# Kernel optimization log

Hardware: AMD Instinct MI355X
Metric: run time of the kernel (lower is better)

Reference implementation:

```python
import jax, jax.numpy as jnp
import numpy as np
from functools import partial

C = 96
D_STATE = 16
D_CONV = 4
EXPAND = 2
D_INNER = EXPAND * C
DT_RANK = (C + 15) // 16  # ceil(96/16) = 6
EPS = 1e-6


def _ln_cf(x, w, b):
    # channels_first LayerNorm over axis=1 of [B,C,D,H,W]
    u = jnp.mean(x, axis=1, keepdims=True)
    s = jnp.mean((x - u) ** 2, axis=1, keepdims=True)
    xn = (x - u) / jnp.sqrt(s + EPS)
    return w[None, :, None, None, None] * xn + b[None, :, None, None, None]


def _ln_last(x, w, b):
    u = jnp.mean(x, axis=-1, keepdims=True)
    s = jnp.mean((x - u) ** 2, axis=-1, keepdims=True)
    return (x - u) / jnp.sqrt(s + 1e-5) * w + b


def _mamba(x, Win, conv_w, conv_b, Wx, Wdt, bdt, A_log, Dp, Wout):
    # x: [B, L, C]
    B, L, _ = x.shape
    xz = jnp.einsum('blc,ec->ble', x, Win)           # [B,L,2*di]
    xin, z = xz[..., :D_INNER], xz[..., D_INNER:]
    # depthwise causal conv along L
    xt = jnp.transpose(xin, (0, 2, 1))               # [B,di,L]
    xt = jnp.pad(xt, ((0, 0), (0, 0), (D_CONV - 1, 0)))
    xc = jax.lax.conv_general_dilated(
        xt, conv_w[:, None, :], window_strides=(1,), padding='VALID',
        feature_group_count=D_INNER, dimension_numbers=('NCH', 'OIH', 'NCH'))
    xc = jax.nn.silu(xc + conv_b[None, :, None])
    xc = jnp.transpose(xc, (0, 2, 1))                # [B,L,di]
    x_dbl = jnp.einsum('bld,ed->ble', xc, Wx)        # [B,L,dt_rank+2*ds]
    dt_r = x_dbl[..., :DT_RANK]
    Bm = x_dbl[..., DT_RANK:DT_RANK + D_STATE]       # [B,L,ds]
    Cm = x_dbl[..., DT_RANK + D_STATE:]              # [B,L,ds]
    dt = jax.nn.softplus(jnp.einsum('blr,dr->bld', dt_r, Wdt) + bdt)
    A = -jnp.exp(A_log)                              # [di,ds]
    dA = jnp.exp(dt[..., None] * A)                  # [B,L,di,ds]
    dBx = (dt * xc)[..., None] * Bm[:, :, None, :]   # [B,L,di,ds]

    def comb(e1, e2):
        a1, b1 = e1
        a2, b2 = e2
        return a1 * a2, a2 * b1 + b2

    _, h = jax.lax.associative_scan(comb, (dA, dBx), axis=1)
    y = jnp.einsum('blds,bls->bld', h, Cm) + xc * Dp
    y = y * jax.nn.silu(z)
    return jnp.einsum('bld,cd->blc', y, Wout)


def setup_inputs() -> dict:
    key = jax.random.key(0)
    ks = jax.random.split(key, 16)
    g = lambda k, sh: jax.random.normal(k, sh, dtype=jnp.float32) * 0.02
    inp = {
        'x': jax.random.normal(ks[0], (2, C, 20, 20, 20), dtype=jnp.float32),
        'ln_w': jnp.ones((C,), jnp.float32), 'ln_b': jnp.zeros((C,), jnp.float32),
        'mln_w': jnp.ones((C,), jnp.float32), 'mln_b': jnp.zeros((C,), jnp.float32),
        'Win': g(ks[1], (2 * D_INNER, C)),
        'conv_w': g(ks[2], (D_INNER, D_CONV)), 'conv_b': jnp.zeros((D_INNER,), jnp.float32),
        'Wx': g(ks[3], (DT_RANK + 2 * D_STATE, D_INNER)),
        'Wdt': g(ks[4], (D_INNER, DT_RANK)), 'bdt': g(ks[5], (D_INNER,)),
        'A_log': jnp.log(jnp.broadcast_to(jnp.arange(1, D_STATE + 1, dtype=jnp.float32), (D_INNER, D_STATE))),
        'Dp': jnp.ones((D_INNER,), jnp.float32),
        'Wout': g(ks[6], (C, D_INNER)),
        'proj_w': g(ks[7], (C, 3 * C)), 'proj_b': jnp.zeros((C,), jnp.float32),
        'fc1_w': g(ks[8], (4 * C, C)), 'fc1_b': jnp.zeros((4 * C,), jnp.float32),
        'fc2_w': g(ks[9], (C, 4 * C)), 'fc2_b': jnp.zeros((C,), jnp.float32),
    }
    return inp


def reference(x, ln_w, ln_b, mln_w, mln_b, Win, conv_w, conv_b, Wx, Wdt, bdt,
              A_log, Dp, Wout, proj_w, proj_b, fc1_w, fc1_b, fc2_w, fc2_b):
    B, Cc, Dd, Hh, Ww = x.shape
    L = Dd * Hh * Ww
    x1 = _ln_cf(x, ln_w, ln_b)
    # three directional flattenings (cube, so reshape shapes match)
    outs = []
    for perm in ((0, 1, 2, 3, 4), (0, 1, 3, 4, 2), (0, 1, 4, 2, 3)):
        xp = jnp.transpose(x1, perm)                     # [B,C,a,b,c]
        xf = jnp.transpose(xp.reshape(B, Cc, L), (0, 2, 1))  # [B,L,C]
        xf = _ln_last(xf, mln_w, mln_b)
        y = _mamba(xf, Win, conv_w, conv_b, Wx, Wdt, bdt, A_log, Dp, Wout)
        outs.append(jnp.transpose(y, (0, 2, 1)).reshape(B, Cc, Dd, Hh, Ww))
    cat = jnp.concatenate(outs, axis=1)                  # [B,3C,D,H,W]
    out1 = jnp.einsum('oc,bcdhw->bodhw', proj_w, cat) + proj_b[None, :, None, None, None]
    out_res = x + out1
    h = _ln_cf(out_res, ln_w, ln_b)
    h = jnp.einsum('oc,bcdhw->bodhw', fc1_w, h) + fc1_b[None, :, None, None, None]
    h = jax.nn.gelu(h, approximate=False)
    h = jnp.einsum('oc,bcdhw->bodhw', fc2_w, h) + fc2_b[None, :, None, None, None]
    return h + out_res
```

## Files before the change

kernel.cpp:

```cpp
#include <hip/hip_runtime.h>
#include <hip/hip_fp16.h>
#include <math.h>

#define S   8000
#define BB  2
#define CC  96
#define DI  192
#define NS  16
#define RK  6
#define GG  6
#define NC  200
#define LC  40
#define ND  38

typedef __attribute__((ext_vector_type(8))) short bf16x8;
typedef __attribute__((ext_vector_type(4))) float f32x4;
typedef __attribute__((ext_vector_type(2))) float f32x2;

__device__ __forceinline__ int pos_from_l(int dir, int l) {
  if (dir == 0) return l;
  int a  = l / 400;
  int r  = l - a * 400;
  int bq = r / 20;
  int cq = r - bq * 20;
  if (dir == 1) return cq * 400 + a * 20 + bq;
  return bq * 400 + cq * 20 + a;
}

__device__ __forceinline__ float silu(float z) {
  return z / (1.f + __expf(-z));
}

__device__ __forceinline__ unsigned short f2bf(float x) {
  unsigned int u = __float_as_uint(x);
  u += 0x7FFFu + ((u >> 16) & 1u);
  return (unsigned short)(u >> 16);
}
__device__ __forceinline__ float bf2f(unsigned short h) {
  return __uint_as_float((unsigned int)h << 16);
}
__device__ __forceinline__ float h2f_bits(unsigned short h) {
  __half hh = *reinterpret_cast<__half*>(&h);
  return __half2float(hh);
}
__device__ __forceinline__ unsigned short f2h_bits(float x) {
  __half hh = __float2half(x);
  return *reinterpret_cast<unsigned short*>(&hh);
}

__device__ __forceinline__ float pair_sum(float y) {
  return y + __int_as_float(__builtin_amdgcn_update_dpp(
      0, __float_as_int(y), 0xB1, 0xF, 0xF, true));
}
__device__ __forceinline__ float quad_sum(float x) {
  x += __int_as_float(__builtin_amdgcn_update_dpp(0, __float_as_int(x), 0xB1, 0xF, 0xF, true));
  x += __int_as_float(__builtin_amdgcn_update_dpp(0, __float_as_int(x), 0x4E, 0xF, 0xF, true));
  return x;
}

template <int ACT, bool DOUBLE, bool OUTBF16>
__global__ __launch_bounds__(256) void k_lnmfma(const float* __restrict__ Xsrc,
    const float* __restrict__ lnw, const float* __restrict__ lnb,
    const float* __restrict__ mlnw, const float* __restrict__ mlnb,
    const float* __restrict__ Bw, const float* __restrict__ bias,
    void* __restrict__ Cout, int M, int N) {
  __shared__ float Xf[64][97];
  __shared__ unsigned short Al[64][104];
  __shared__ unsigned short Bl[96][104];
  int tid = threadIdx.x;
  int m0 = blockIdx.x * 64, n0 = blockIdx.y * 96;
  int b = m0 / S, pos0 = m0 - b * S;
  for (int idx = tid; idx < 64 * 96; idx += 256) {
    int row = idx & 63, c = idx >> 6;
    Xf[row][c] = Xsrc[((size_t)b * CC + c) * S + pos0 + row];
  }
  for (int idx = tid; idx < 96 * 24; idx += 256) {
    int bn = idx / 24, kq = idx - bn * 24;
    int n = n0 + bn;
    float4 v = make_float4(0.f, 0.f, 0.f, 0.f);
    if (n < N) v = *(const float4*)&Bw[(size_t)n * 96 + kq * 4];
    unsigned short* dst = &Bl[bn][kq * 4];
    dst[0] = f2bf(v.x); dst[1] = f2bf(v.y);
    dst[2] = f2bf(v.z); dst[3] = f2bf(v.w);
  }
  __syncthreads();
  {
    int row = tid >> 2, part = tid & 3;
    const float* xr = &Xf[row][part * 24];
    float s1 = 0.f, s2 = 0.f;
#pragma unroll
    for (int i = 0; i < 24; ++i) { float v = xr[i]; s1 += v; s2 += v * v; }
    s1 = quad_sum(s1); s2 = quad_sum(s2);
    float u = s1 * (1.f / 96.f);
    float var = s2 * (1.f / 96.f) - u * u;
    float rstd = rsqrtf(var + 1e-6f);
    if (DOUBLE) {
      float t1 = 0.f, t2 = 0.f;
#pragma unroll
      for (int i = 0; i < 24; ++i) {
        int c = part * 24 + i;
        float y1 = fmaf(lnw[c], (xr[i] - u) * rstd, lnb[c]);
        t1 += y1; t2 += y1 * y1;
      }
      t1 = quad_sum(t1); t2 = quad_sum(t2);
      float u2 = t1 * (1.f / 96.f);
      float var2 = t2 * (1.f / 96.f) - u2 * u2;
      float rstd2 = rsqrtf(var2 + 1e-5f);
#pragma unroll
      for (int i = 0; i < 24; ++i) {
        int c = part * 24 + i;
        float y1 = fmaf(lnw[c], (xr[i] - u) * rstd, lnb[c]);
        Al[row][c] = f2bf(fmaf(mlnw[c], (y1 - u2) * rstd2, mlnb[c]));
      }
    } else {
#pragma unroll
      for (int i = 0; i < 24; ++i) {
        int c = part * 24 + i;
        Al[row][c] = f2bf(fmaf(lnw[c], (xr[i] - u) * rstd, lnb[c]));
      }
    }
  }
  __syncthreads();
  int wid = tid >> 6, lane = tid & 63;
  int wr = wid >> 1, wc = wid & 1;
  int l16 = lane & 15, lk = (lane >> 4) * 8;
  f32x4 acc[2][3];
#pragma unroll
  for (int i = 0; i < 2; ++i)
#pragma unroll
    for (int j = 0; j < 3; ++j) acc[i][j] = (f32x4){0.f, 0.f, 0.f, 0.f};
#pragma unroll
  for (int kc = 0; kc < 96; kc += 32) {
    bf16x8 af[2], bfr[3];
#pragma unroll
    for (int i = 0; i < 2; ++i)
      af[i] = *(const bf16x8*)&Al[wr * 32 + i * 16 + l16][kc + lk];
#pragma unroll
    for (int j = 0; j < 3; ++j)
      bfr[j] = *(const bf16x8*)&Bl[wc * 48 + j * 16 + l16][kc + lk];
#pragma unroll
    for (int i = 0; i < 2; ++i)
#pragma unroll
      for (int j = 0; j < 3; ++j)
        acc[i][j] = __builtin_amdgcn_mfma_f32_16x16x32_bf16(
            af[i], bfr[j], acc[i][j], 0, 0, 0);
  }
#pragma unroll
  for (int i = 0; i < 2; ++i) {
#pragma unroll
    for (int j = 0; j < 3; ++j) {
#pragma unroll
      for (int v = 0; v < 4; ++v) {
        int m = m0 + wr * 32 + i * 16 + (lane >> 4) * 4 + v;
        int n = n0 + wc * 48 + j * 16 + l16;
        if (n < N) {
          float val = acc[i][j][v];
          val += bias ? bias[n] : 0.f;
          if (ACT == 1) val = 0.5f * val * (1.f + erff(val * 0.70710678118654752f));
          if (OUTBF16) ((unsigned short*)Cout)[(size_t)m * N + n] = f2bf(val);
          else         ((float*)Cout)[(size_t)m * N + n] = val;
        }
      }
    }
  }
}

#define BKP 40
template <int ACT, bool BIAS, bool RESID, bool OUT_BCS, bool GATEA, bool ABF16>
__global__ __launch_bounds__(256) void k_mfma(const void* __restrict__ Ap,
    const float* __restrict__ Bw, const float* __restrict__ bias,
    const float* __restrict__ resid, const unsigned short* __restrict__ XZg,
    float* __restrict__ Cmat, int M, int N, int K) {
  __shared__ unsigned short Al[64][BKP];
  __shared__ unsigned short Bl[96][BKP];
  int tid = threadIdx.x;
  int m0 = blockIdx.x * 64, n0 = blockIdx.y * 96;
  int wid = tid >> 6, lane = tid & 63;
  int wr = wid >> 1, wc = wid & 1;
  int l16 = lane & 15, lk = (lane >> 4) * 8;
  f32x4 acc[2][3];
#pragma unroll
  for (int i = 0; i < 2; ++i)
#pragma unroll
    for (int j = 0; j < 3; ++j) acc[i][j] = (f32x4){0.f, 0.f, 0.f, 0.f};

  for (int kk = 0; kk < K; kk += 32) {
    if (ABF16) {
      int row = tid >> 2, kq = tid & 3;
      int m = m0 + row;
      const unsigned short* As = (const unsigned short*)Ap;
      uint4 v = *(const uint4*)&As[(size_t)m * K + kk + kq * 8];
      if (GATEA) {
        unsigned short* pv = (unsigned short*)&v;
        int bb = m / S, ll = m - bb * S;
        int j = kk + kq * 8;
        int dir = j / DI; int e0 = j - dir * DI;
        int p = pos_from_l(dir, ll);
        uint4 zv = *(const uint4*)&XZg[((size_t)bb * S + p) * 384 + DI + e0];
        const unsigned short* zp = (const unsigned short*)&zv;
#pragma unroll
        for (int q = 0; q < 8; ++q)
          pv[q] = f2bf(bf2f(pv[q]) * silu(bf2f(zp[q])));
      }
      *(uint4*)&Al[row][kq * 8] = v;
    } else {
#pragma unroll
      for (int i = 0; i < 2; ++i) {
        int idx = tid + i * 256;
        int row = idx >> 3, kq = idx & 7;
        int m = m0 + row;
        const float* Af = (const float*)Ap;
        float4 v = *(const float4*)&Af[(size_t)m * K + kk + kq * 4];
        unsigned short* dst = &Al[row][kq * 4];
        dst[0] = f2bf(v.x); dst[1] = f2bf(v.y);
        dst[2] = f2bf(v.z); dst[3] = f2bf(v.w);
      }
    }
#pragma unroll
    for (int i = 0; i < 3; ++i) {
      int idx = tid + i * 256;
      int bn = idx >> 3, kq = idx & 7;
      int n = n0 + bn;
      float4 v = make_float4(0.f, 0.f, 0.f, 0.f);
      if (n < N) v = *(const float4*)&Bw[(size_t)n * K + kk + kq * 4];
      unsigned short* dst = &Bl[bn][kq * 4];
      dst[0] = f2bf(v.x); dst[1] = f2bf(v.y);
      dst[2] = f2bf(v.z); dst[3] = f2bf(v.w);
    }
    __syncthreads();
    bf16x8 af[2], bfr[3];
#pragma unroll
    for (int i = 0; i < 2; ++i)
      af[i] = *(const bf16x8*)&Al[wr * 32 + i * 16 + l16][lk];
#pragma unroll
    for (int j = 0; j < 3; ++j)
      bfr[j] = *(const bf16x8*)&Bl[wc * 48 + j * 16 + l16][lk];
#pragma unroll
    for (int i = 0; i < 2; ++i)
#pragma unroll
      for (int j = 0; j < 3; ++j)
        acc[i][j] = __builtin_amdgcn_mfma_f32_16x16x32_bf16(
            af[i], bfr[j], acc[i][j], 0, 0, 0);
    __syncthreads();
  }
#pragma unroll
  for (int i = 0; i < 2; ++i) {
#pragma unroll
    for (int j = 0; j < 3; ++j) {
#pragma unroll
      for (int v = 0; v < 4; ++v) {
        int m = m0 + wr * 32 + i * 16 + (lane >> 4) * 4 + v;
        int n = n0 + wc * 48 + j * 16 + l16;
        if (n < N) {
          float val = acc[i][j][v];
          if (BIAS) val += bias[n];
          if (ACT == 1) val = 0.5f * val * (1.f + erff(val * 0.70710678118654752f));
          if (RESID || OUT_BCS) {
            int bb = m / S, pp = m - bb * S;
            size_t oidx = ((size_t)bb * CC + n) * S + pp;
            if (RESID) val += resid[oidx];
            if (OUT_BCS) { Cmat[oidx] = val; continue; }
          }
          Cmat[(size_t)m * N + n] = val;
        }
      }
    }
  }
}

__global__ __launch_bounds__(256) void k_conv(const unsigned short* __restrict__ XZb,
    const float* __restrict__ cw, const float* __restrict__ cb,
    unsigned short* __restrict__ xcb) {
  int t = blockIdx.x * blockDim.x + threadIdx.x;
  if (t >= GG * S * 48) return;
  int q = t % 48; int gl = t / 48; int l = gl % S; int g = gl / S;
  int e0 = q * 4;
  int b = g / 3, dir = g - (g / 3) * 3;
  float cwv[4][4];
#pragma unroll
  for (int i = 0; i < 4; ++i)
    *(float4*)cwv[i] = *(const float4*)&cw[(e0 + i) * 4];
  float4 acc = *(const float4*)&cb[e0];
#pragma unroll
  for (int k = 0; k < 4; ++k) {
    int ls = l + k - 3;
    if (ls >= 0) {
      int p = pos_from_l(dir, ls);
      uint2 xz = *(const uint2*)&XZb[((size_t)b * S + p) * 384 + e0];
      const unsigned short* xp = (const unsigned short*)&xz;
      acc.x = fmaf(cwv[0][k], bf2f(xp[0]), acc.x);
      acc.y = fmaf(cwv[1][k], bf2f(xp[1]), acc.y);
      acc.z = fmaf(cwv[2][k], bf2f(xp[2]), acc.z);
      acc.w = fmaf(cwv[3][k], bf2f(xp[3]), acc.w);
    }
  }
  unsigned short o[4];
  o[0] = f2bf(acc.x * (1.f / (1.f + __expf(-acc.x))));
  o[1] = f2bf(acc.y * (1.f / (1.f + __expf(-acc.y))));
  o[2] = f2bf(acc.z * (1.f / (1.f + __expf(-acc.z))));
  o[3] = f2bf(acc.w * (1.f / (1.f + __expf(-acc.w))));
  *(uint2*)&xcb[(size_t)gl * DI + e0] = *(uint2*)o;
}

__global__ __launch_bounds__(256) void k_dtr(const float* __restrict__ xdbl,
    const float* __restrict__ Wdt, const float* __restrict__ bdt,
    const float* __restrict__ A_log, unsigned int* __restrict__ dr) {
  int t = blockIdx.x * blockDim.x + threadIdx.x;
  if (t >= GG * S * DI) return;
  int e = t % DI; int row = t / DI;
  const float* xr = xdbl + (size_t)row * ND;
  float a = bdt[e];
#pragma unroll
  for (int r = 0; r < RK; ++r) a = fmaf(Wdt[e * RK + r], xr[r], a);
  float d = fmaxf(a, 0.f) + __logf(1.f + __expf(-fabsf(a)));
  float base = -__expf(A_log[e * NS]);
  unsigned int lo = f2h_bits(d);
  unsigned int hi = f2h_bits(__expf(d * base));
  dr[t] = lo | (hi << 16);
}

__device__ __forceinline__ void stage_b16(float (*sB)[16],
    const float* __restrict__ xdbl, int g, int c, int tid) {
  const float* src = xdbl + ((size_t)g * S + c * LC) * ND + RK;
  for (int i = tid; i < LC * 16; i += 192) {
    int row = i >> 4, col = i & 15;
    sB[row][col] = src[(size_t)row * ND + col];
  }
}
__device__ __forceinline__ void stage_bc32(float (*sBC)[32],
    const float* __restrict__ xdbl, int g, int c, int tid) {
  const float* src = xdbl + ((size_t)g * S + c * LC) * ND + RK;
  for (int i = tid; i < LC * 32; i += 192) {
    int row = i >> 5, col = i & 31;
    sBC[row][col] = src[(size_t)row * ND + col];
  }
}

__global__ __launch_bounds__(192) void k_scanA(const unsigned short* __restrict__ xcb,
    const unsigned int* __restrict__ dr,
    const float* __restrict__ xdbl, const float* __restrict__ A_log,
    float* __restrict__ PA, float* __restrict__ EA) {
  __shared__ float sB[LC][16];
  int c = blockIdx.x, g = blockIdx.y;
  int tid = threadIdx.x;
  int e = blockIdx.z * 96 + (tid >> 1);
  int hf = tid & 1;
  stage_b16(sB, xdbl, g, c, tid);
  float base = -__expf(A_log[e * NS]);
  bool fast = true;
#pragma unroll
  for (int s = 1; s < NS; ++s) {
    float aes = -__expf(A_log[e * NS + s]);
    fast = fast && (fabsf(aes / base - (float)(s + 1)) < 1e-3f);
  }
  f32x2 h2[4];
#pragma unroll
  for (int k = 0; k < 4; ++k) h2[k] = (f32x2){0.f, 0.f};
  float T = 0.f;
  size_t sbase = ((size_t)g * S + c * LC) * DI + e;
  const unsigned short* xp = xcb + sbase;
  const unsigned int* drp = dr + sbase;
  __syncthreads();
  if (fast) {
    for (int l0 = 0; l0 < LC; l0 += 8) {
      float xb[8], db[8], rv[8];
#pragma unroll
      for (int j = 0; j < 8; ++j) {
        xb[j] = bf2f(xp[(size_t)(l0 + j) * DI]);
        unsigned int v = drp[(size_t)(l0 + j) * DI];
        db[j] = h2f_bits((unsigned short)(v & 0xffff));
        rv[j] = h2f_bits((unsigned short)(v >> 16));
      }
#pragma unroll
      for (int j = 0; j < 8; ++j) {
        int l = l0 + j;
        float d = db[j];
        T += d;
        float w = d * xb[j];
        float r = rv[j];
        float r2 = r * r, r4 = r2 * r2, r8 = r4 * r4;
        float f = hf ? r8 * r : r;
        f32x2 m0 = {f, f * r};
        f32x2 m1 = m0 * (f32x2){r2, r2};
        f32x2 m2 = m0 * (f32x2){r4, r4};
        f32x2 m3 = m1 * (f32x2){r4, r4};
        f32x2 wv = {w, w};
        float4 Ba = *(const float4*)&sB[l][hf * 8];
        float4 Bb = *(const float4*)&sB[l][hf * 8 + 4];
        h2[0] = m0 * h2[0] + wv * (f32x2){Ba.x, Ba.y};
        h2[1] = m1 * h2[1] + wv * (f32x2){Ba.z, Ba.w};
        h2[2] = m2 * h2[2] + wv * (f32x2){Bb.x, Bb.y};
        h2[3] = m3 * h2[3] + wv * (f32x2){Bb.z, Bb.w};
      }
    }
  } else {
    float Aes[8];
#pragma unroll
    for (int k = 0; k < 8; ++k) Aes[k] = -__expf(A_log[e * NS + hf * 8 + k]);
#pragma unroll 1
    for (int l = 0; l < LC; ++l) {
      unsigned int v = drp[(size_t)l * DI];
      float d = h2f_bits((unsigned short)(v & 0xffff));
      T += d;
      float w = d * bf2f(xp[(size_t)l * DI]);
#pragma unroll
      for (int k = 0; k < 8; ++k) {
        float q = __expf(d * Aes[k]);
        h2[k >> 1][k & 1] = fmaf(q, h2[k >> 1][k & 1], w * sB[l][hf * 8 + k]);
      }
    }
  }
  float* pp = PA + (((size_t)g * NC + c) * DI + e) * NS + hf * 8;
  float* ep = EA + (((size_t)g * NC + c) * DI + e) * NS + hf * 8;
  float po[8];
  if (fast) {
    float r = __expf(base * T);
    float r2 = r * r, r4 = r2 * r2, r8 = r4 * r4;
    float f = hf ? r8 * r : r;
    po[0] = f; po[1] = f * r; po[2] = f * r2; po[3] = po[1] * r2;
    po[4] = f * r4; po[5] = po[1] * r4; po[6] = po[2] * r4; po[7] = po[3] * r4;
  } else {
#pragma unroll
    for (int k = 0; k < 8; ++k)
      po[k] = __expf(-__expf(A_log[e * NS + hf * 8 + k]) * T);
  }
  *(float4*)&pp[0] = make_float4(po[0], po[1], po[2], po[3]);
  *(float4*)&pp[4] = make_float4(po[4], po[5], po[6], po[7]);
  *(float4*)&ep[0] = make_float4(h2[0][0], h2[0][1], h2[1][0], h2[1][1]);
  *(float4*)&ep[4] = make_float4(h2[2][0], h2[2][1], h2[3][0], h2[3][1]);
}

__global__ __launch_bounds__(256) void k_scanB(const float* PA,
    const float* EA, float* Hin) {
  int idx = blockIdx.x * blockDim.x + threadIdx.x;
  if (idx >= GG * DI * NS) return;
  int g = idx / (DI * NS); int es = idx - g * (DI * NS);
  size_t stride = (size_t)DI * NS;
  size_t b0 = (size_t)g * NC * stride + es;
  float h = 0.f;
  for (int c0 = 0; c0 < NC; c0 += 8) {
    float p8[8], e8[8];
#pragma unroll
    for (int j = 0; j < 8; ++j) {
      size_t ix = b0 + (size_t)(c0 + j) * stride;
      p8[j] = PA[ix]; e8[j] = EA[ix];
    }
#pragma unroll
    for (int j = 0; j < 8; ++j) {
      size_t ix = b0 + (size_t)(c0 + j) * stride;
      Hin[ix] = h;
      h = fmaf(p8[j], h, e8[j]);
    }
  }
}

__global__ __launch_bounds__(192) void k_scanC(const unsigned short* __restrict__ xcb,
    const unsigned int* __restrict__ dr,
    const float* __restrict__ xdbl, const float* __restrict__ A_log,
    const float* __restrict__ Hin, const float* __restrict__ Dp,
    unsigned short* __restrict__ ygb) {
  __shared__ float sBC[LC][32];
  int c = blockIdx.x, g = blockIdx.y;
  int tid = threadIdx.x;
  int e = blockIdx.z * 96 + (tid >> 1);
  int hf = tid & 1;
  const float* hp = Hin + (((size_t)g * NC + c) * DI + e) * NS + hf * 8;
  float4 h0 = *(const float4*)(hp + 0);
  float4 h1v = *(const float4*)(hp + 4);
  stage_bc32(sBC, xdbl, g, c, tid);
  float dpe = Dp[e];
  float base = -__expf(A_log[e * NS]);
  bool fast = true;
#pragma unroll
  for (int s = 1; s < NS; ++s) {
    float aes = -__expf(A_log[e * NS + s]);
    fast = fast && (fabsf(aes / base - (float)(s + 1)) < 1e-3f);
  }
  f32x2 h2[4] = {{h0.x, h0.y}, {h0.z, h0.w}, {h1v.x, h1v.y}, {h1v.z, h1v.w}};
  size_t sbase = ((size_t)g * S + c * LC) * DI + e;
  const unsigned short* xp = xcb + sbase;
  const unsigned int* drp = dr + sbase;
  int b = g / 3, dir = g - (g / 3) * 3;
  unsigned short* yo = ygb + ((size_t)b * S + c * LC) * 576 + dir * DI + e;
  __syncthreads();
  if (fast) {
    for (int l0 = 0; l0 < LC; l0 += 8) {
      float xb[8], db[8], rv[8];
#pragma unroll
      for (int j = 0; j < 8; ++j) {
        xb[j] = bf2f(xp[(size_t)(l0 + j) * DI]);
        unsigned int v = drp[(size_t)(l0 + j) * DI];
        db[j] = h2f_bits((unsigned short)(v & 0xffff));
        rv[j] = h2f_bits((unsigned short)(v >> 16));
      }
#pragma unroll
      for (int j = 0; j < 8; ++j) {
        int l = l0 + j;
        float d = db[j];
        float xv = xb[j];
        float w = d * xv;
        float r = rv[j];
        float r2 = r * r, r4 = r2 * r2, r8 = r4 * r4;
        float f = hf ? r8 * r : r;
        f32x2 m0 = {f, f * r};
        f32x2 m1 = m0 * (f32x2){r2, r2};
        f32x2 m2 = m0 * (f32x2){r4, r4};
        f32x2 m3 = m1 * (f32x2){r4, r4};
        f32x2 wv = {w, w};
        float4 Ba = *(const float4*)&sBC[l][hf * 8];
        float4 Bb = *(const float4*)&sBC[l][hf * 8 + 4];
        float4 Ca = *(const float4*)&sBC[l][16 + hf * 8];
        float4 Cb = *(const float4*)&sBC[l][16 + hf * 8 + 4];
        f32x2 yacc = {hf ? 0.f : xv * dpe, 0.f};
        h2[0] = m0 * h2[0] + wv * (f32x2){Ba.x, Ba.y};
        yacc += h2[0] * (f32x2){Ca.x, Ca.y};
        h2[1] = m1 * h2[1] + wv * (f32x2){Ba.z, Ba.w};
        yacc += h2[1] * (f32x2){Ca.z, Ca.w};
        h2[2] = m2 * h2[2] + wv * (f32x2){Bb.x, Bb.y};
        yacc += h2[2] * (f32x2){Cb.x, Cb.y};
        h2[3] = m3 * h2[3] + wv * (f32x2){Bb.z, Bb.w};
        yacc += h2[3] * (f32x2){Cb.z, Cb.w};
        float ysum = pair_sum(yacc[0] + yacc[1]);
        if (!hf) yo[(size_t)l * 576] = f2bf(ysum);
      }
    }
  } else {
    float Aes[8];
#pragma unroll
    for (int k = 0; k < 8; ++k) Aes[k] = -__expf(A_log[e * NS + hf * 8 + k]);
#pragma unroll 1
    for (int l = 0; l < LC; ++l) {
      unsigned int v = drp[(size_t)l * DI];
      float d = h2f_bits((unsigned short)(v & 0xffff));
      float xv = bf2f(xp[(size_t)l * DI]);
      float w = d * xv;
      float y = hf ? 0.f : xv * dpe;
#pragma unroll
      for (int k = 0; k < 8; ++k) {
        float q = __expf(d * Aes[k]);
        float hk = fmaf(q, h2[k >> 1][k & 1], w * sBC[l][hf * 8 + k]);
        h2[k >> 1][k & 1] = hk;
        y = fmaf(hk, sBC[l][16 + hf * 8 + k], y);
      }
      float ysum = pair_sum(y);
      if (!hf) yo[(size_t)l * 576] = f2bf(ysum);
    }
  }
}

__global__ __launch_bounds__(256) void k_foldW(const float* __restrict__ proj_w,
    const float* __restrict__ Wout, float* __restrict__ Mcat) {
  int t = blockIdx.x * blockDim.x + threadIdx.x;
  if (t >= CC * 576) return;
  int o = t / 576; int j = t - o * 576; int dir = j / DI; int e = j - dir * DI;
  float a = 0.f;
  for (int c2 = 0; c2 < CC; ++c2)
    a = fmaf(proj_w[o * 288 + dir * CC + c2], Wout[c2 * DI + e], a);
  Mcat[t] = a;
}

extern "C" void kernel_launch(void* const* d_in, const int* in_sizes, int n_in,
                              void* d_out, int out_size, void* d_ws, size_t ws_size,
                              hipStream_t stream) {
  const float* x      = (const float*)d_in[0];
  const float* ln_w   = (const float*)d_in[1];
  const float* ln_b   = (const float*)d_in[2];
  const float* mln_w  = (const float*)d_in[3];
  const float* mln_b  = (const float*)d_in[4];
  const float* Win    = (const float*)d_in[5];
  const float* conv_w = (const float*)d_in[6];
  const float* conv_b = (const float*)d_in[7];
  const float* Wx     = (const float*)d_in[8];
  const float* Wdt    = (const float*)d_in[9];
  const float* bdt    = (const float*)d_in[10];
  const float* A_log  = (const float*)d_in[11];
  const float* Dp     = (const float*)d_in[12];
  const float* Wout   = (const float*)d_in[13];
  const float* proj_w = (const float*)d_in[14];
  const float* proj_b = (const float*)d_in[15];
  const float* fc1_w  = (const float*)d_in[16];
  const float* fc1_b  = (const float*)d_in[17];
  const float* fc2_w  = (const float*)d_in[18];
  const float* fc2_b  = (const float*)d_in[19];

  float* ws = (float*)d_ws;
  size_t off = 0;
  float* ores = ws + off; off += (size_t)BB * S * CC;
  float* XZf  = ws + off; off += (size_t)BB * S * 384 / 2;
  float* xcf  = ws + off; off += (size_t)GG * S * DI / 2;
  float* xdbl = ws + off; off += (size_t)GG * S * ND;
  float* drf  = ws + off; off += (size_t)GG * S * DI;
  float* PA   = ws + off; off += (size_t)GG * NC * DI * NS;
  float* EA   = ws + off; off += (size_t)GG * NC * DI * NS;
  float* yg   = ws + off; off += (size_t)BB * S * 576 / 2;
  float* Mcat = ws + off; off += (size_t)CC * 576;
  if (ws_size < off * sizeof(float)) return;
  float* Hin  = PA;
  unsigned short* XZb = (unsigned short*)XZf;
  unsigned short* xcb = (unsigned short*)xcf;
  unsigned int*   dr  = (unsigned int*)drf;
  unsigned short* ygb = (unsigned short*)yg;
  unsigned short* h1  = (unsigned short*)XZf;

  k_lnmfma<0, true, true><<<dim3(BB * S / 64, 4), 256, 0, stream>>>(
      x, ln_w, ln_b, mln_w, mln_b, Win, nullptr, XZb, BB * S, 384);
  k_conv<<<(GG * S * 48 + 255) / 256, 256, 0, stream>>>(XZb, conv_w, conv_b, xcb);
  k_mfma<0, false, false, false, false, true>
      <<<dim3(GG * S / 64, 1), 256, 0, stream>>>(
      xcb, Wx, nullptr, nullptr, nullptr, xdbl, GG * S, ND, DI);
  k_dtr<<<(GG * S * DI + 255) / 256, 256, 0, stream>>>(
      xdbl, Wdt, bdt, A_log, dr);
  k_scanA<<<dim3(NC, GG, 2), 192, 0, stream>>>(
      xcb, dr, xdbl, A_log, PA, EA);
  k_scanB<<<(GG * DI * NS + 255) / 256, 256, 0, stream>>>(PA, EA, Hin);
  k_scanC<<<dim3(NC, GG, 2), 192, 0, stream>>>(
      xcb, dr, xdbl, A_log, Hin, Dp, ygb);
  k_foldW<<<(CC * 576 + 255) / 256, 256, 0, stream>>>(proj_w, Wout, Mcat);
  k_mfma<0, true, true, true, true, true>
      <<<dim3(BB * S / 64, 1), 256, 0, stream>>>(
      ygb, Mcat, proj_b, x, XZb, ores, BB * S, CC, 576);
  k_lnmfma<1, false, true><<<dim3(BB * S / 64, 4), 256, 0, stream>>>(
      ores, ln_w, ln_b, nullptr, nullptr, fc1_w, fc1_b, h1, BB * S, 384);
  k_mfma<0, true, true, true, false, true>
      <<<dim3(BB * S / 64, 1), 256, 0, stream>>>(
      h1, fc2_w, fc2_b, ores, nullptr, (float*)d_out, BB * S, CC, 384);
}
```

Baseline: 286.4 us.

## Compute local scan output in pass A and apply carry-in correction in pass C

The chunked selective scan is restructured. The first pass now computes the full per-chunk local output y (with zero initial state), stores it along with a half-precision running cumulative dt, and uses one thread per channel over all 16 states instead of two half-threads. The third pass no longer re-runs the recurrence. It only adds the decayed carry-in contribution, using exp(A*T) derived from the stored cumulative sum, and skips wavefronts whose incoming state is all zero. k_dtr is also vectorised to produce four channels per thread with a 16-byte store. The trade-offs are an extra buffer write and read-modify-write of y, fp16 precision for the cumulative T, and fewer threads per block in pass A.

After: 258.8 us. 1.11x faster.

```diff
diff --git a/kernel.cpp b/kernel.cpp
--- a/kernel.cpp
+++ b/kernel.cpp
@@ -30,7 +30,6 @@
 __device__ __forceinline__ float silu(float z) {
   return z / (1.f + __expf(-z));
 }
-
 __device__ __forceinline__ unsigned short f2bf(float x) {
   unsigned int u = __float_as_uint(x);
   u += 0x7FFFu + ((u >> 16) & 1u);
@@ -46,11 +45,6 @@
 __device__ __forceinline__ unsigned short f2h_bits(float x) {
   __half hh = __float2half(x);
   return *reinterpret_cast<unsigned short*>(&hh);
-}
-
-__device__ __forceinline__ float pair_sum(float y) {
-  return y + __int_as_float(__builtin_amdgcn_update_dpp(
-      0, __float_as_int(y), 0xB1, 0xF, 0xF, true));
 }
 __device__ __forceinline__ float quad_sum(float x) {
   x += __int_as_float(__builtin_amdgcn_update_dpp(0, __float_as_int(x), 0xB1, 0xF, 0xF, true));
@@ -306,46 +300,42 @@
     const float* __restrict__ Wdt, const float* __restrict__ bdt,
     const float* __restrict__ A_log, unsigned int* __restrict__ dr) {
   int t = blockIdx.x * blockDim.x + threadIdx.x;
-  if (t >= GG * S * DI) return;
-  int e = t % DI; int row = t / DI;
+  if (t >= GG * S * 48) return;
+  int q = t % 48; int row = t / 48;
+  int e0 = q * 4;
   const float* xr = xdbl + (size_t)row * ND;
-  float a = bdt[e];
-#pragma unroll
-  for (int r = 0; r < RK; ++r) a = fmaf(Wdt[e * RK + r], xr[r], a);
-  float d = fmaxf(a, 0.f) + __logf(1.f + __expf(-fabsf(a)));
-  float base = -__expf(A_log[e * NS]);
-  unsigned int lo = f2h_bits(d);
-  unsigned int hi = f2h_bits(__expf(d * base));
-  dr[t] = lo | (hi << 16);
-}
-
-__device__ __forceinline__ void stage_b16(float (*sB)[16],
-    const float* __restrict__ xdbl, int g, int c, int tid) {
-  const float* src = xdbl + ((size_t)g * S + c * LC) * ND + RK;
-  for (int i = tid; i < LC * 16; i += 192) {
-    int row = i >> 4, col = i & 15;
-    sB[row][col] = src[(size_t)row * ND + col];
-  }
-}
-__device__ __forceinline__ void stage_bc32(float (*sBC)[32],
-    const float* __restrict__ xdbl, int g, int c, int tid) {
-  const float* src = xdbl + ((size_t)g * S + c * LC) * ND + RK;
-  for (int i = tid; i < LC * 32; i += 192) {
-    int row = i >> 5, col = i & 31;
-    sBC[row][col] = src[(size_t)row * ND + col];
-  }
-}
-
-__global__ __launch_bounds__(192) void k_scanA(const unsigned short* __restrict__ xcb,
-    const unsigned int* __restrict__ dr,
-    const float* __restrict__ xdbl, const float* __restrict__ A_log,
-    float* __restrict__ PA, float* __restrict__ EA) {
-  __shared__ float sB[LC][16];
+  float r0 = xr[0], r1 = xr[1], r2 = xr[2], r3 = xr[3], r4 = xr[4], r5 = xr[5];
+  unsigned int out[4];
+#pragma unroll
+  for (int i = 0; i < 4; ++i) {
+    int e = e0 + i;
+    const float* wp = &Wdt[e * RK];
+    float a = bdt[e];
+    a = fmaf(wp[0], r0, a); a = fmaf(wp[1], r1, a); a = fmaf(wp[2], r2, a);
+    a = fmaf(wp[3], r3, a); a = fmaf(wp[4], r4, a); a = fmaf(wp[5], r5, a);
+    float d = fmaxf(a, 0.f) + __logf(1.f + __expf(-fabsf(a)));
+    float base = -__expf(A_log[e * NS]);
+    out[i] = (unsigned int)f2h_bits(d) | ((unsigned int)f2h_bits(__expf(d * base)) << 16);
+  }
+  *(uint4*)&dr[(size_t)row * DI + e0] = *(uint4*)out;
+}
+
+__global__ __launch_bounds__(192) void k_scanA2(const unsigned short* __restrict__ xcb,
+    const unsigned int* __restrict__ dr, const float* __restrict__ xdbl,
+    const float* __restrict__ A_log, const float* __restrict__ Dp,
+    float* __restrict__ PA, float* __restrict__ EA,
+    unsigned short* __restrict__ Tb, unsigned short* __restrict__ ygb) {
+  __shared__ float sBC[LC][32];
   int c = blockIdx.x, g = blockIdx.y;
   int tid = threadIdx.x;
-  int e = blockIdx.z * 96 + (tid >> 1);
-  int hf = tid & 1;
-  stage_b16(sB, xdbl, g, c, tid);
+  int e = tid;
+  {
+    const float* src = xdbl + ((size_t)g * S + c * LC) * ND + RK;
+    for (int i = tid; i < LC * 32; i += 192) {
+      int row = i >> 5, col = i & 31;
+      sBC[row][col] = src[(size_t)row * ND + col];
+    }
+  }
   float base = -__expf(A_log[e * NS]);
   bool fast = true;
 #pragma unroll
@@ -353,81 +343,115 @@
     float aes = -__expf(A_log[e * NS + s]);
     fast = fast && (fabsf(aes / base - (float)(s + 1)) < 1e-3f);
   }
-  f32x2 h2[4];
-#pragma unroll
-  for (int k = 0; k < 4; ++k) h2[k] = (f32x2){0.f, 0.f};
+  float dpe = Dp[e];
+  f32x2 h2[8];
+#pragma unroll
+  for (int k = 0; k < 8; ++k) h2[k] = (f32x2){0.f, 0.f};
   float T = 0.f;
   size_t sbase = ((size_t)g * S + c * LC) * DI + e;
   const unsigned short* xp = xcb + sbase;
   const unsigned int* drp = dr + sbase;
+  unsigned short* Tp = Tb + sbase;
+  int b = g / 3, dir = g - (g / 3) * 3;
+  unsigned short* yo = ygb + ((size_t)b * S + c * LC) * 576 + dir * DI + e;
   __syncthreads();
   if (fast) {
-    for (int l0 = 0; l0 < LC; l0 += 8) {
-      float xb[8], db[8], rv[8];
+    unsigned short xb[2][8];
+    unsigned int dv[2][8];
+#pragma unroll
+    for (int j = 0; j < 8; ++j) {
+      xb[0][j] = xp[(size_t)j * DI];
+      dv[0][j] = drp[(size_t)j * DI];
+    }
+#pragma unroll
+    for (int blk = 0; blk < 5; ++blk) {
+      int cb = blk & 1, nb = cb ^ 1;
+      if (blk < 4) {
+#pragma unroll
+        for (int j = 0; j < 8; ++j) {
+          xb[nb][j] = xp[(size_t)(blk * 8 + 8 + j) * DI];
+          dv[nb][j] = drp[(size_t)(blk * 8 + 8 + j) * DI];
+        }
+      }
 #pragma unroll
       for (int j = 0; j < 8; ++j) {
-        xb[j] = bf2f(xp[(size_t)(l0 + j) * DI]);
-        unsigned int v = drp[(size_t)(l0 + j) * DI];
-        db[j] = h2f_bits((unsigned short)(v & 0xffff));
-        rv[j] = h2f_bits((unsigned short)(v >> 16));
-      }
-#pragma unroll
-      for (int j = 0; j < 8; ++j) {
-        int l = l0 + j;
-        float d = db[j];
+        int l = blk * 8 + j;
+        float xv = bf2f(xb[cb][j]);
+        unsigned int v = dv[cb][j];
+        float d = h2f_bits((unsigned short)(v & 0xffff));
+        float r = h2f_bits((unsigned short)(v >> 16));
         T += d;
-        float w = d * xb[j];
-        float r = rv[j];
+        Tp[(size_t)l * DI] = f2h_bits(T);
+        float w = d * xv;
         float r2 = r * r, r4 = r2 * r2, r8 = r4 * r4;
-        float f = hf ? r8 * r : r;
-        f32x2 m0 = {f, f * r};
-        f32x2 m1 = m0 * (f32x2){r2, r2};
-        f32x2 m2 = m0 * (f32x2){r4, r4};
-        f32x2 m3 = m1 * (f32x2){r4, r4};
+        f32x2 r2v = {r2, r2}, r4v = {r4, r4}, r8v = {r8, r8};
+        f32x2 m0 = {r, r2};
+        f32x2 m1 = m0 * r2v, m2 = m0 * r4v, m3 = m1 * r4v;
+        f32x2 m4 = m0 * r8v, m5 = m1 * r8v, m6 = m2 * r8v, m7 = m3 * r8v;
         f32x2 wv = {w, w};
-        float4 Ba = *(const float4*)&sB[l][hf * 8];
-        float4 Bb = *(const float4*)&sB[l][hf * 8 + 4];
-        h2[0] = m0 * h2[0] + wv * (f32x2){Ba.x, Ba.y};
-        h2[1] = m1 * h2[1] + wv * (f32x2){Ba.z, Ba.w};
-        h2[2] = m2 * h2[2] + wv * (f32x2){Bb.x, Bb.y};
-        h2[3] = m3 * h2[3] + wv * (f32x2){Bb.z, Bb.w};
+        float4 Ba = *(const float4*)&sBC[l][0];
+        float4 Bb = *(const float4*)&sBC[l][4];
+        float4 Bc = *(const float4*)&sBC[l][8];
+        float4 Bd = *(const float4*)&sBC[l][12];
+        float4 Ca = *(const float4*)&sBC[l][16];
+        float4 Cb2 = *(const float4*)&sBC[l][20];
+        float4 Cc = *(const float4*)&sBC[l][24];
+        float4 Cd = *(const float4*)&sBC[l][28];
+        f32x2 ya = {xv * dpe, 0.f};
+        h2[0] = m0 * h2[0] + wv * (f32x2){Ba.x, Ba.y}; ya += h2[0] * (f32x2){Ca.x, Ca.y};
+        h2[1] = m1 * h2[1] + wv * (f32x2){Ba.z, Ba.w}; ya += h2[1] * (f32x2){Ca.z, Ca.w};
+        h2[2] = m2 * h2[2] + wv * (f32x2){Bb.x, Bb.y}; ya += h2[2] * (f32x2){Cb2.x, Cb2.y};
+        h2[3] = m3 * h2[3] + wv * (f32x2){Bb.z, Bb.w}; ya += h2[3] * (f32x2){Cb2.z, Cb2.w};
+        h2[4] = m4 * h2[4] + wv * (f32x2){Bc.x, Bc.y}; ya += h2[4] * (f32x2){Cc.x, Cc.y};
+        h2[5] = m5 * h2[5] + wv * (f32x2){Bc.z, Bc.w}; ya += h2[5] * (f32x2){Cc.z, Cc.w};
+        h2[6] = m6 * h2[6] + wv * (f32x2){Bd.x, Bd.y}; ya += h2[6] * (f32x2){Cd.x, Cd.y};
+        h2[7] = m7 * h2[7] + wv * (f32x2){Bd.z, Bd.w}; ya += h2[7] * (f32x2){Cd.z, Cd.w};
+        yo[(size_t)l * 576] = f2bf(ya[0] + ya[1]);
       }
     }
   } else {
-    float Aes[8];
-#pragma unroll
-    for (int k = 0; k < 8; ++k) Aes[k] = -__expf(A_log[e * NS + hf * 8 + k]);
+    float Aes[NS];
+#pragma unroll
+    for (int s = 0; s < NS; ++s) Aes[s] = -__expf(A_log[e * NS + s]);
 #pragma unroll 1
     for (int l = 0; l < LC; ++l) {
       unsigned int v = drp[(size_t)l * DI];
       float d = h2f_bits((unsigned short)(v & 0xffff));
+      float xv = bf2f(xp[(size_t)l * DI]);
       T += d;
-      float w = d * bf2f(xp[(size_t)l * DI]);
-#pragma unroll
-      for (int k = 0; k < 8; ++k) {
-        float q = __expf(d * Aes[k]);
-        h2[k >> 1][k & 1] = fmaf(q, h2[k >> 1][k & 1], w * sB[l][hf * 8 + k]);
-      }
-    }
-  }
-  float* pp = PA + (((size_t)g * NC + c) * DI + e) * NS + hf * 8;
-  float* ep = EA + (((size_t)g * NC + c) * DI + e) * NS + hf * 8;
-  float po[8];
+      Tp[(size_t)l * DI] = f2h_bits(T);
+      float w = d * xv;
+      float y = xv * dpe;
+#pragma unroll
+      for (int s = 0; s < NS; ++s) {
+        float q = __expf(d * Aes[s]);
+        float hk = fmaf(q, h2[s >> 1][s & 1], w * sBC[l][s]);
+        h2[s >> 1][s & 1] = hk;
+        y = fmaf(hk, sBC[l][16 + s], y);
+      }
+      yo[(size_t)l * 576] = f2bf(y);
+    }
+  }
+  float* pp = PA + (((size_t)g * NC + c) * DI + e) * NS;
+  float* ep = EA + (((size_t)g * NC + c) * DI + e) * NS;
+  float po[NS];
   if (fast) {
-    float r = __expf(base * T);
-    float r2 = r * r, r4 = r2 * r2, r8 = r4 * r4;
-    float f = hf ? r8 * r : r;
-    po[0] = f; po[1] = f * r; po[2] = f * r2; po[3] = po[1] * r2;
-    po[4] = f * r4; po[5] = po[1] * r4; po[6] = po[2] * r4; po[7] = po[3] * r4;
+    float R = __expf(base * T);
+    float R2 = R * R, R4 = R2 * R2, R8 = R4 * R4;
+    po[0] = R; po[1] = R2; po[2] = R * R2; po[3] = R4;
+    po[4] = R4 * R; po[5] = R4 * R2; po[6] = po[5] * R; po[7] = R8;
+    po[8] = R8 * R; po[9] = R8 * R2; po[10] = po[9] * R; po[11] = R8 * R4;
+    po[12] = po[11] * R; po[13] = po[11] * R2; po[14] = po[13] * R; po[15] = R8 * R8;
   } else {
 #pragma unroll
-    for (int k = 0; k < 8; ++k)
-      po[k] = __expf(-__expf(A_log[e * NS + hf * 8 + k]) * T);
-  }
-  *(float4*)&pp[0] = make_float4(po[0], po[1], po[2], po[3]);
-  *(float4*)&pp[4] = make_float4(po[4], po[5], po[6], po[7]);
-  *(float4*)&ep[0] = make_float4(h2[0][0], h2[0][1], h2[1][0], h2[1][1]);
-  *(float4*)&ep[4] = make_float4(h2[2][0], h2[2][1], h2[3][0], h2[3][1]);
+    for (int s = 0; s < NS; ++s)
+      po[s] = __expf(-__expf(A_log[e * NS + s]) * T);
+  }
+#pragma unroll
+  for (int s = 0; s < NS; s += 4) {
+    *(float4*)&pp[s] = make_float4(po[s], po[s+1], po[s+2], po[s+3]);
+    *(float4*)&ep[s] = make_float4(h2[s>>1][0], h2[s>>1][1], h2[(s>>1)+1][0], h2[(s>>1)+1][1]);
+  }
 }
 
 __global__ __launch_bounds__(256) void k_scanB(const float* PA,
@@ -454,21 +478,20 @@
   }
 }
 
-__global__ __launch_bounds__(192) void k_scanC(const unsigned short* __restrict__ xcb,
-    const unsigned int* __restrict__ dr,
+__global__ __launch_bounds__(192) void k_scanC2(const unsigned short* __restrict__ Tb,
     const float* __restrict__ xdbl, const float* __restrict__ A_log,
-    const float* __restrict__ Hin, const float* __restrict__ Dp,
-    unsigned short* __restrict__ ygb) {
-  __shared__ float sBC[LC][32];
+    const float* __restrict__ Hin, unsigned short* __restrict__ ygb) {
+  __shared__ float sC[LC][16];
   int c = blockIdx.x, g = blockIdx.y;
   int tid = threadIdx.x;
-  int e = blockIdx.z * 96 + (tid >> 1);
-  int hf = tid & 1;
-  const float* hp = Hin + (((size_t)g * NC + c) * DI + e) * NS + hf * 8;
-  float4 h0 = *(const float4*)(hp + 0);
-  float4 h1v = *(const float4*)(hp + 4);
-  stage_bc32(sBC, xdbl, g, c, tid);
-  float dpe = Dp[e];
+  int e = tid;
+  {
+    const float* src = xdbl + ((size_t)g * S + c * LC) * ND + RK + 16;
+    for (int i = tid; i < LC * 16; i += 192) {
+      int row = i >> 4, col = i & 15;
+      sC[row][col] = src[(size_t)row * ND + col];
+    }
+  }
   float base = -__expf(A_log[e * NS]);
   bool fast = true;
 #pragma unroll
@@ -476,74 +499,80 @@
     float aes = -__expf(A_log[e * NS + s]);
     fast = fast && (fabsf(aes / base - (float)(s + 1)) < 1e-3f);
   }
-  f32x2 h2[4] = {{h0.x, h0.y}, {h0.z, h0.w}, {h1v.x, h1v.y}, {h1v.z, h1v.w}};
+  const float* hp = Hin + (((size_t)g * NC + c) * DI + e) * NS;
+  float4 hv0 = *(const float4*)(hp + 0);
+  float4 hv1 = *(const float4*)(hp + 4);
+  float4 hv2 = *(const float4*)(hp + 8);
+  float4 hv3 = *(const float4*)(hp + 12);
+  f32x2 hin[8] = {{hv0.x, hv0.y}, {hv0.z, hv0.w}, {hv1.x, hv1.y}, {hv1.z, hv1.w},
+                  {hv2.x, hv2.y}, {hv2.z, hv2.w}, {hv3.x, hv3.y}, {hv3.z, hv3.w}};
+  float hmag = fabsf(hv0.x) + fabsf(hv0.y) + fabsf(hv0.z) + fabsf(hv0.w) +
+               fabsf(hv1.x) + fabsf(hv1.y) + fabsf(hv1.z) + fabsf(hv1.w) +
+               fabsf(hv2.x) + fabsf(hv2.y) + fabsf(hv2.z) + fabsf(hv2.w) +
+               fabsf(hv3.x) + fabsf(hv3.y) + fabsf(hv3.z) + fabsf(hv3.w);
   size_t sbase = ((size_t)g * S + c * LC) * DI + e;
-  const unsigned short* xp = xcb + sbase;
-  const unsigned int* drp = dr + sbase;
+  const unsigned short* Tp = Tb + sbase;
   int b = g / 3, dir = g - (g / 3) * 3;
   unsigned short* yo = ygb + ((size_t)b * S + c * LC) * 576 + dir * DI + e;
   __syncthreads();
+  if (__builtin_amdgcn_ballot_w64(hmag != 0.f) == 0ull) return;
   if (fast) {
-    for (int l0 = 0; l0 < LC; l0 += 8) {
-      float xb[8], db[8], rv[8];
+    unsigned short tb2[2][8], yb[2][8];
+#pragma unroll
+    for (int j = 0; j < 8; ++j) {
+      tb2[0][j] = Tp[(size_t)j * DI];
+      yb[0][j] = yo[(size_t)j * 576];
+    }
+#pragma unroll
+    for (int blk = 0; blk < 5; ++blk) {
+      int cb = blk & 1, nb = cb ^ 1;
+      if (blk < 4) {
+#pragma unroll
+        for (int j = 0; j < 8; ++j) {
+          tb2[nb][j] = Tp[(size_t)(blk * 8 + 8 + j) * DI];
+          yb[nb][j] = yo[(size_t)(blk * 8 + 8 + j) * 576];
+        }
+      }
 #pragma unroll
       for (int j = 0; j < 8; ++j) {
-        xb[j] = bf2f(xp[(size_t)(l0 + j) * DI]);
-        unsigned int v = drp[(size_t)(l0 + j) * DI];
-        db[j] = h2f_bits((unsigned short)(v & 0xffff));
-        rv[j] = h2f_bits((unsigned short)(v >> 16));
-      }
-#pragma unroll
-      for (int j = 0; j < 8; ++j) {
-        int l = l0 + j;
-        float d = db[j];
-        float xv = xb[j];
-        float w = d * xv;
-        float r = rv[j];
-        float r2 = r * r, r4 = r2 * r2, r8 = r4 * r4;
-        float f = hf ? r8 * r : r;
-        f32x2 m0 = {f, f * r};
-        f32x2 m1 = m0 * (f32x2){r2, r2};
-        f32x2 m2 = m0 * (f32x2){r4, r4};
-        f32x2 m3 = m1 * (f32x2){r4, r4};
-        f32x2 wv = {w, w};
-        float4 Ba = *(const float4*)&sBC[l][hf * 8];
-        float4 Bb = *(const float4*)&sBC[l][hf * 8 + 4];
-        float4 Ca = *(const float4*)&sBC[l][16 + hf * 8];
-        float4 Cb = *(const float4*)&sBC[l][16 + hf * 8 + 4];
-        f32x2 yacc = {hf ? 0.f : xv * dpe, 0.f};
-        h2[0] = m0 * h2[0] + wv * (f32x2){Ba.x, Ba.y};
-        yacc += h2[0] * (f32x2){Ca.x, Ca.y};
-        h2[1] = m1 * h2[1] + wv * (f32x2){Ba.z, Ba.w};
-        yacc += h2[1] * (f32x2){Ca.z, Ca.w};
-        h2[2] = m2 * h2[2] + wv * (f32x2){Bb.x, Bb.y};
-        yacc += h2[2] * (f32x2){Cb.x, Cb.y};
-        h2[3] = m3 * h2[3] + wv * (f32x2){Bb.z, Bb.w};
-        yacc += h2[3] * (f32x2){Cb.z, Cb.w};
-        float ysum = pair_sum(yacc[0] + yacc[1]);
-        if (!hf) yo[(size_t)l * 576] = f2bf(ysum);
+        int l = blk * 8 + j;
+        float T = h2f_bits(tb2[cb][j]);
+        float R = __expf(base * T);
+        float R2 = R * R, R4 = R2 * R2, R8 = R4 * R4;
+        f32x2 R2v = {R2, R2}, R4v = {R4, R4}, R8v = {R8, R8};
+        f32x2 q0 = {R, R2};
+        f32x2 q1 = q0 * R2v, q2 = q0 * R4v, q3 = q1 * R4v;
+        f32x2 q4 = q0 * R8v, q5 = q1 * R8v, q6 = q2 * R8v, q7 = q3 * R8v;
+        float4 Ca = *(const float4*)&sC[l][0];
+        float4 Cb2 = *(const float4*)&sC[l][4];
+        float4 Cc = *(const float4*)&sC[l][8];
+        float4 Cd = *(const float4*)&sC[l][12];
+        f32x2 ca = (hin[0] * q0) * (f32x2){Ca.x, Ca.y};
+        ca += (hin[1] * q1) * (f32x2){Ca.z, Ca.w};
+        ca += (hin[2] * q2) * (f32x2){Cb2.x, Cb2.y};
+        ca += (hin[3] * q3) * (f32x2){Cb2.z, Cb2.w};
+        ca += (hin[4] * q4) * (f32x2){Cc.x, Cc.y};
+        ca += (hin[5] * q5) * (f32x2){Cc.z, Cc.w};
+        ca += (hin[6] * q6) * (f32x2){Cd.x, Cd.y};
+        ca += (hin[7] * q7) * (f32x2){Cd.z, Cd.w};
+        float y = bf2f(yb[cb][j]) + ca[0] + ca[1];
+        yo[(size_t)l * 576] = f2bf(y);
       }
     }
   } else {
-    float Aes[8];
-#pragma unroll
-    for (int k = 0; k < 8; ++k) Aes[k] = -__expf(A_log[e * NS + hf * 8 + k]);
+    float Aes[NS];
+#pragma unroll
+    for (int s = 0; s < NS; ++s) Aes[s] = -__expf(A_log[e * NS + s]);
 #pragma unroll 1
     for (int l = 0; l < LC; ++l) {
-      unsigned int v = drp[(size_t)l * DI];
-      float d = h2f_bits((unsigned short)(v & 0xffff));
-      float xv = bf2f(xp[(size_t)l * DI]);
-      float w = d * xv;
-      float y = hf ? 0.f : xv * dpe;
-#pragma unroll
-      for (int k = 0; k < 8; ++k) {
-        float q = __expf(d * Aes[k]);
-        float hk = fmaf(q, h2[k >> 1][k & 1], w * sBC[l][hf * 8 + k]);
-        h2[k >> 1][k & 1] = hk;
-        y = fmaf(hk, sBC[l][16 + hf * 8 + k], y);
-      }
-      float ysum = pair_sum(y);
-      if (!hf) yo[(size_t)l * 576] = f2bf(ysum);
+      float T = h2f_bits(Tp[(size_t)l * DI]);
+      float y = bf2f(yo[(size_t)l * 576]);
+#pragma unroll
+      for (int s = 0; s < NS; ++s) {
+        float W = __expf(Aes[s] * T);
+        y = fmaf(hin[s >> 1][s & 1] * W, sC[l][s], y);
+      }
+      yo[(size_t)l * 576] = f2bf(y);
     }
   }
 }
@@ -590,6 +619,7 @@
   float* xcf  = ws + off; off += (size_t)GG * S * DI / 2;
   float* xdbl = ws + off; off += (size_t)GG * S * ND;
   float* drf  = ws + off; off += (size_t)GG * S * DI;
+  float* Tf   = ws + off; off += (size_t)GG * S * DI / 2;
   float* PA   = ws + off; off += (size_t)GG * NC * DI * NS;
   float* EA   = ws + off; off += (size_t)GG * NC * DI * NS;
   float* yg   = ws + off; off += (size_t)BB * S * 576 / 2;
@@ -599,6 +629,7 @@
   unsigned short* XZb = (unsigned short*)XZf;
   unsigned short* xcb = (unsigned short*)xcf;
   unsigned int*   dr  = (unsigned int*)drf;
+  unsigned short* Tb  = (unsigned short*)Tf;
   unsigned short* ygb = (unsigned short*)yg;
   unsigned short* h1  = (unsigned short*)XZf;
 
@@ -608,13 +639,13 @@
   k_mfma<0, false, false, false, false, true>
       <<<dim3(GG * S / 64, 1), 256, 0, stream>>>(
       xcb, Wx, nullptr, nullptr, nullptr, xdbl, GG * S, ND, DI);
-  k_dtr<<<(GG * S * DI + 255) / 256, 256, 0, stream>>>(
+  k_dtr<<<(GG * S * 48 + 255) / 256, 256, 0, stream>>>(
       xdbl, Wdt, bdt, A_log, dr);
-  k_scanA<<<dim3(NC, GG, 2), 192, 0, stream>>>(
-      xcb, dr, xdbl, A_log, PA, EA);
+  k_scanA2<<<dim3(NC, GG), 192, 0, stream>>>(
+      xcb, dr, xdbl, A_log, Dp, PA, EA, Tb, ygb);
   k_scanB<<<(GG * DI * NS + 255) / 256, 256, 0, stream>>>(PA, EA, Hin);
-  k_scanC<<<dim3(NC, GG, 2), 192, 0, stream>>>(
-      xcb, dr, xdbl, A_log, Hin, Dp, ygb);
+  k_scanC2<<<dim3(NC, GG), 192, 0, stream>>>(
+      Tb, xdbl, A_log, Hin, ygb);
   k_foldW<<<(CC * 576 + 255) / 256, 256, 0, stream>>>(proj_w, Wout, Mcat);
   k_mfma<0, true, true, true, true, true>
       <<<dim3(BB * S / 64, 1), 256, 0, stream>>>(
```
